# Kernel optimization log

Hardware: AMD Instinct MI355X
Metric: run time of the kernel (lower is better)

## Reference

```python
import jax, jax.numpy as jnp
import numpy as np

K = 3
PAD = 1
DG = 4
GN_GROUPS = 32
EPS = 1e-5


def deform_conv2d(x, offset, weight):
    # x: [B,C,H,W], offset: [B,DG*2*K*K,H,W] (mmcv layout: per group, per kernel tap, (dy,dx))
    B, C, H, W = x.shape
    KK = K * K
    cg = C // DG
    dt = x.dtype
    off = offset.reshape(B, DG, KK, 2, H, W)
    dy, dx = off[:, :, :, 0], off[:, :, :, 1]  # [B,DG,KK,H,W]
    ky, kx = jnp.meshgrid(jnp.arange(K), jnp.arange(K), indexing='ij')
    ky = ky.reshape(KK).astype(dt)
    kx = kx.reshape(KK).astype(dt)
    hh = jnp.arange(H, dtype=dt)
    ww = jnp.arange(W, dtype=dt)
    # sampling coords: p0 + p_k + offset (stride 1, dilation 1)
    y = hh[None, None, None, :, None] - PAD + ky[None, None, :, None, None] + dy
    xs = ww[None, None, None, None, :] - PAD + kx[None, None, :, None, None] + dx
    y0 = jnp.floor(y)
    x0 = jnp.floor(xs)
    wy1 = y - y0
    wx1 = xs - x0
    xg = x.reshape(B, DG, cg, H * W)

    def corner(yi, xi):
        # zero padding outside the feature map
        valid = (yi >= 0) & (yi < H) & (xi >= 0) & (xi < W)
        yc = jnp.clip(yi, 0, H - 1).astype(jnp.int32)
        xc = jnp.clip(xi, 0, W - 1).astype(jnp.int32)
        idx = (yc * W + xc).reshape(B, DG, KK * H * W)
        v = jax.vmap(jax.vmap(lambda xf, ix: xf[:, ix]))(xg, idx)  # [B,DG,cg,KK*H*W]
        v = v.reshape(B, DG, cg, KK, H, W)
        return v * valid.astype(dt)[:, :, None]

    col = (corner(y0, x0) * ((1 - wy1) * (1 - wx1))[:, :, None]
           + corner(y0, x0 + 1) * ((1 - wy1) * wx1)[:, :, None]
           + corner(y0 + 1, x0) * (wy1 * (1 - wx1))[:, :, None]
           + corner(y0 + 1, x0 + 1) * (wy1 * wx1)[:, :, None])  # [B,DG,cg,KK,H,W]
    col = col.reshape(B, C, KK, H, W)
    O = weight.shape[0]
    return jnp.einsum('ock,bckhw->bohw', weight.reshape(O, C, KK), col)


def group_norm(x, gamma, beta):
    B, C, H, W = x.shape
    xg = x.reshape(B, GN_GROUPS, -1)
    m = xg.mean(-1, keepdims=True)
    v = xg.var(-1, keepdims=True)
    xn = ((xg - m) * jax.lax.rsqrt(v + EPS)).reshape(B, C, H, W)
    return xn * gamma[None, :, None, None] + beta[None, :, None, None]


def setup_inputs() -> dict:
    key = jax.random.key(0)
    k1, k2, k3, k4 = jax.random.split(key, 4)
    B, C, H, W = 4, 256, 64, 64
    x = jax.random.normal(k1, (B, C, H, W), dtype=jnp.float32)
    shape = jax.random.normal(k2, (B, 4, H, W), dtype=jnp.float32)
    w_offset = jax.random.normal(k3, (DG * 2 * K * K, 4), dtype=jnp.float32) * 0.01
    w_deform = jax.random.normal(k4, (C, C, K, K), dtype=jnp.float32) * 0.01
    gamma = jnp.ones((C,), jnp.float32)
    beta = jnp.zeros((C,), jnp.float32)
    return {"x": x, "shape": shape, "w_offset": w_offset, "w_deform": w_deform, "gamma": gamma, "beta": beta}


def reference(x, shape, w_offset, w_deform, gamma, beta):
    # conv_offset: 1x1 conv on detached `shape`
    offset = jnp.einsum('oi,bihw->bohw', w_offset, jax.lax.stop_gradient(shape))
    out = deform_conv2d(x, offset, w_deform)
    return jax.nn.relu(group_norm(out, gamma, beta))
```

## Files before the change

kernel.cpp:

```cpp
#include <hip/hip_runtime.h>
#include <stdint.h>

#define BB   4
#define CCH  256
#define HH   64
#define WWD  64
#define HWSZ 4096
#define DGRP 4
#define CG   64
#define KKN  9
#define KT   2304
#define NND  16384
#define GNG  32
#define EPSV 1e-5f

#define WS_COLT  0
#define WS_WB    75497472
#define WS_G     76677120
#define WS_STATS 93454336
#define WS_PART  93455360

typedef __attribute__((ext_vector_type(8))) short short8;
typedef __attribute__((ext_vector_type(4))) float f32x4;

__device__ inline unsigned short f2bf(float f) {
    union { float f; unsigned u; } v; v.f = f;
    unsigned u = v.u;
    return (unsigned short)((u + 0x7FFFu + ((u >> 16) & 1u)) >> 16);
}

__device__ inline void gl_lds16(const void* g, void* l) {
    __builtin_amdgcn_global_load_lds(
        (const __attribute__((address_space(1))) void*)g,
        (__attribute__((address_space(3))) void*)l,
        16, 0, 0);
}

__global__ __launch_bounds__(256) void wconv_kernel(const float* __restrict__ wd,
                                                    unsigned short* __restrict__ Wb) {
    int idx = blockIdx.x * 256 + threadIdx.x;
    int o = idx / KT;
    int r = idx % KT;
    int kk = r >> 8;
    int c  = r & 255;
    Wb[idx] = f2bf(wd[o * KT + c * KKN + kk]);
}

__global__ __launch_bounds__(256) void col_kernel(const float* __restrict__ x,
                                                  const float* __restrict__ shp,
                                                  const float* __restrict__ woff,
                                                  unsigned short* __restrict__ colT) {
    __shared__ __align__(16) float xt[8 * 8 * 64 * 4];

    int bid   = blockIdx.x;
    int band  = bid & 15;
    int chalf = (bid >> 4) & 1;
    int dg    = (bid >> 5) & 3;
    int b     = bid >> 7;
    int h0    = band * 4;
    int tid   = threadIdx.x;
    int lane  = tid & 63;
    int wv    = tid >> 6;

    const float* xg = x + (size_t)(b * CCH + dg * CG + chalf * 32) * HWSZ;
    #pragma unroll 1
    for (int ii = 0; ii < 8; ++ii) {
        float v[8]; int la[8];
        #pragma unroll
        for (int u = 0; u < 8; ++u) {
            int idx = (ii * 8 + u) * 256 + tid;
            int w = idx & 63;
            int r = (idx >> 6) & 7;
            int j = idx >> 9;
            int gr = min(max(h0 - 2 + r, 0), HH - 1);
            v[u]  = xg[(size_t)j * HWSZ + gr * 64 + w];
            la[u] = ((j >> 2) * 8 + r) * 256 + w * 4 + (j & 3);
        }
        #pragma unroll
        for (int u = 0; u < 8; ++u) xt[la[u]] = v[u];
    }
    __syncthreads();

    int h  = h0 + wv;
    int hw = h * 64 + lane;
    float s0 = shp[(b * 4 + 0) * HWSZ + hw];
    float s1 = shp[(b * 4 + 1) * HWSZ + hw];
    float s2 = shp[(b * 4 + 2) * HWSZ + hw];
    float s3 = shp[(b * 4 + 3) * HWSZ + hw];

    unsigned short* rowp = colT + (size_t)(b * HWSZ + hw) * KT + dg * CG + chalf * 32;
    const char* xtb = (const char*)xt;

    #pragma unroll
    for (int kk = 0; kk < KKN; ++kk) {
        const float* wo = woff + (dg * 18 + kk * 2) * 4;
        float dy = wo[0] * s0 + wo[1] * s1 + wo[2] * s2 + wo[3] * s3;
        float dx = wo[4] * s0 + wo[5] * s1 + wo[6] * s2 + wo[7] * s3;

        int ky = kk / 3, kx = kk % 3;
        float y  = (float)(h - 1 + ky) + dy;
        float xs = (float)(lane - 1 + kx) + dx;
        float y0f = floorf(y), x0f = floorf(xs);
        float wy1 = y - y0f,  wx1 = xs - x0f;
        float wy0 = 1.f - wy1, wx0 = 1.f - wx1;
        int iy0 = (int)y0f, ix0 = (int)x0f;
        int iy1 = iy0 + 1,  ix1 = ix0 + 1;
        bool vy0 = (iy0 >= 0) && (iy0 < HH);
        bool vy1 = (iy1 >= 0) && (iy1 < HH);
        bool vx0 = (ix0 >= 0) && (ix0 < WWD);
        bool vx1 = (ix1 >= 0) && (ix1 < WWD);
        float w00 = (vy0 && vx0) ? wy0 * wx0 : 0.f;
        float w01 = (vy0 && vx1) ? wy0 * wx1 : 0.f;
        float w10 = (vy1 && vx0) ? wy1 * wx0 : 0.f;
        float w11 = (vy1 && vx1) ? wy1 * wx1 : 0.f;
        int cy0 = min(max(iy0, 0), HH - 1);
        int cy1 = min(max(iy1, 0), HH - 1);
        int cx0 = min(max(ix0, 0), WWD - 1);
        int cx1 = min(max(ix1, 0), WWD - 1);
        int ty0 = min(max(cy0 - (h0 - 2), 0), 7);
        int ty1 = min(max(cy1 - (h0 - 2), 0), 7);
        int a00 = (ty0 * 64 + cx0) * 16;
        int a01 = (ty0 * 64 + cx1) * 16;
        int a10 = (ty1 * 64 + cx0) * 16;
        int a11 = (ty1 * 64 + cx1) * 16;

        unsigned short tmp[32];
        #pragma unroll
        for (int c4g = 0; c4g < 8; ++c4g) {
            int base = c4g * 8192;
            const float4 v00 = *(const float4*)(xtb + base + a00);
            const float4 v01 = *(const float4*)(xtb + base + a01);
            const float4 v10 = *(const float4*)(xtb + base + a10);
            const float4 v11 = *(const float4*)(xtb + base + a11);
            float rx = w00 * v00.x + w01 * v01.x + w10 * v10.x + w11 * v11.x;
            float ry = w00 * v00.y + w01 * v01.y + w10 * v10.y + w11 * v11.y;
            float rz = w00 * v00.z + w01 * v01.z + w10 * v10.z + w11 * v11.z;
            float rw = w00 * v00.w + w01 * v01.w + w10 * v10.w + w11 * v11.w;
            tmp[c4g * 4 + 0] = f2bf(rx);
            tmp[c4g * 4 + 1] = f2bf(ry);
            tmp[c4g * 4 + 2] = f2bf(rz);
            tmp[c4g * 4 + 3] = f2bf(rw);
        }
        uint4* dst = (uint4*)(rowp + kk * 256);
        const uint4* src = (const uint4*)tmp;
        dst[0] = src[0];
        dst[1] = src[1];
        dst[2] = src[2];
        dst[3] = src[3];
    }
}

__global__ __launch_bounds__(256) void gemm_kernel(const unsigned short* __restrict__ Wb,
                                                   const unsigned short* __restrict__ colT,
                                                   float* __restrict__ G) {
    __shared__ __align__(16) short As[64 * 32];
    __shared__ __align__(16) short Bs[128 * 32];

    int tid  = threadIdx.x;
    int lane = tid & 63;
    int wv   = tid >> 6;
    int wm   = wv >> 1;
    int wn   = wv & 1;
    int m0   = (blockIdx.x & 3) * 64;
    int n0   = (blockIdx.x >> 2) * 128;

    int erow = tid >> 2;
    int ecol = (tid & 3) * 8;
    const unsigned short* gA = Wb   + (size_t)(m0 + erow) * KT + ecol;
    const unsigned short* gB = colT + (size_t)(n0 + erow) * KT + ecol;
    short* lA = As + tid * 8;
    short* lB = Bs + tid * 8;

    f32x4 acc[2][4] = {};

    int quad = lane >> 4;
    int lrow = lane & 15;

    for (int kt = 0; kt < KT; kt += 32) {
        gl_lds16(gA + kt,            lA);
        gl_lds16(gB + kt,            lB);
        gl_lds16(gB + 64 * KT + kt,  lB + 2048);
        __syncthreads();

        short8 a[2], b[4];
        #pragma unroll
        for (int i = 0; i < 2; ++i)
            a[i] = *(const short8*)&As[(wm * 32 + i * 16 + lrow) * 32 + quad * 8];
        #pragma unroll
        for (int j = 0; j < 4; ++j)
            b[j] = *(const short8*)&Bs[(wn * 64 + j * 16 + lrow) * 32 + quad * 8];
        #pragma unroll
        for (int i = 0; i < 2; ++i)
            #pragma unroll
            for (int j = 0; j < 4; ++j)
                acc[i][j] = __builtin_amdgcn_mfma_f32_16x16x32_bf16(a[i], b[j], acc[i][j], 0, 0, 0);
        __syncthreads();
    }

    #pragma unroll
    for (int i = 0; i < 2; ++i) {
        int m = m0 + wm * 32 + i * 16 + quad * 4;
        #pragma unroll
        for (int j = 0; j < 4; ++j) {
            int n = n0 + wn * 64 + j * 16 + lrow;
            #pragma unroll
            for (int r = 0; r < 4; ++r)
                G[(size_t)(m + r) * NND + n] = acc[i][j][r];
        }
    }
}

__global__ __launch_bounds__(256) void gn_part_kernel(const float* __restrict__ G,
                                                      float* __restrict__ partials) {
    int blk = blockIdx.x;
    int bg  = blk >> 3;
    int o   = blk & 7;
    int b   = bg >> 5;
    int g   = bg & 31;
    const float* row = G + (size_t)(g * 8 + o) * NND + b * HWSZ;
    float s1 = 0.f, s2 = 0.f;
    #pragma unroll
    for (int it = 0; it < 16; ++it) {
        float v = row[it * 256 + threadIdx.x];
        s1 += v;
        s2 += v * v;
    }
    #pragma unroll
    for (int off = 1; off < 64; off <<= 1) {
        s1 += __shfl_xor(s1, off);
        s2 += __shfl_xor(s2, off);
    }
    __shared__ float red[8];
    if ((threadIdx.x & 63) == 0) {
        red[(threadIdx.x >> 6) * 2]     = s1;
        red[(threadIdx.x >> 6) * 2 + 1] = s2;
    }
    __syncthreads();
    if (threadIdx.x == 0) {
        partials[blk * 2]     = red[0] + red[2] + red[4] + red[6];
        partials[blk * 2 + 1] = red[1] + red[3] + red[5] + red[7];
    }
}

__global__ __launch_bounds__(128) void gn_stats_kernel(const float* __restrict__ partials,
                                                       float* __restrict__ stats) {
    int bg = threadIdx.x;
    float t1 = 0.f, t2 = 0.f;
    #pragma unroll
    for (int o = 0; o < 8; ++o) {
        t1 += partials[(bg * 8 + o) * 2];
        t2 += partials[(bg * 8 + o) * 2 + 1];
    }
    const float invN = 1.f / 32768.f;
    float mean = t1 * invN;
    float var  = t2 * invN - mean * mean;
    stats[bg * 2]     = mean;
    stats[bg * 2 + 1] = rsqrtf(var + EPSV);
}

__global__ __launch_bounds__(256) void gn_apply_kernel(const float* __restrict__ G,
                                                       const float* __restrict__ stats,
                                                       const float* __restrict__ gamma,
                                                       const float* __restrict__ beta,
                                                       float* __restrict__ out) {
    int idx = blockIdx.x * 256 + threadIdx.x;
    int hw4 = idx & 1023;
    int o   = (idx >> 10) & 255;
    int b   = idx >> 18;
    int g   = o >> 3;
    float mean = stats[(b * 32 + g) * 2];
    float rstd = stats[(b * 32 + g) * 2 + 1];
    float ga = gamma[o], be = beta[o];
    const float4 v = *(const float4*)&G[(size_t)o * NND + b * HWSZ + hw4 * 4];
    float4 r;
    r.x = fmaxf(0.f, (v.x - mean) * rstd * ga + be);
    r.y = fmaxf(0.f, (v.y - mean) * rstd * ga + be);
    r.z = fmaxf(0.f, (v.z - mean) * rstd * ga + be);
    r.w = fmaxf(0.f, (v.w - mean) * rstd * ga + be);
    *(float4*)&out[(size_t)(b * CCH + o) * HWSZ + hw4 * 4] = r;
}

extern "C" void kernel_launch(void* const* d_in, const int* in_sizes, int n_in,
                              void* d_out, int out_size, void* d_ws, size_t ws_size,
                              hipStream_t stream) {
    const float* x     = (const float*)d_in[0];
    const float* shp   = (const float*)d_in[1];
    const float* woff  = (const float*)d_in[2];
    const float* wdef  = (const float*)d_in[3];
    const float* gamma = (const float*)d_in[4];
    const float* beta  = (const float*)d_in[5];
    float* out = (float*)d_out;

    char* ws = (char*)d_ws;
    unsigned short* colT = (unsigned short*)(ws + WS_COLT);
    unsigned short* Wb   = (unsigned short*)(ws + WS_WB);
    float* G             = (float*)(ws + WS_G);
    float* stats         = (float*)(ws + WS_STATS);
    float* partials      = (float*)(ws + WS_PART);

    wconv_kernel<<<2304, 256, 0, stream>>>(wdef, Wb);
    col_kernel<<<512, 256, 0, stream>>>(x, shp, woff, colT);
    gemm_kernel<<<512, 256, 0, stream>>>(Wb, colT, G);
    gn_part_kernel<<<1024, 256, 0, stream>>>(G, partials);
    gn_stats_kernel<<<1, 128, 0, stream>>>(partials, stats);
    gn_apply_kernel<<<4096, 256, 0, stream>>>(G, stats, gamma, beta, out);
}
```

Before: 164.5 us.

## Retile deform-conv GEMM to full-M 256x64 blocks with K-step 64

The GEMM block now covers all 256 output channels and 64 columns, using 512 threads (8 waves in a 4x2 layout) and a K-step of 64, so each colT column tile is loaded only once instead of four times. The weight tile is reloaded per block, which is cheaper because the weights are small and cache-resident. Halving the number of K iterations also halves the barrier count. In exchange, the grid drops to 256 blocks, which may underfill a 256-CU device, and LDS use grows to about 40KB per block.

```diff
diff --git a/kernel.cpp b/kernel.cpp
--- a/kernel.cpp
+++ b/kernel.cpp
@@ -150,59 +150,61 @@
     }
 }
 
-__global__ __launch_bounds__(256) void gemm_kernel(const unsigned short* __restrict__ Wb,
+__global__ __launch_bounds__(512) void gemm_kernel(const unsigned short* __restrict__ Wb,
                                                    const unsigned short* __restrict__ colT,
                                                    float* __restrict__ G) {
-    __shared__ __align__(16) short As[64 * 32];
-    __shared__ __align__(16) short Bs[128 * 32];
+    __shared__ __align__(16) short As[256 * 64];
+    __shared__ __align__(16) short Bs[64 * 64];
 
     int tid  = threadIdx.x;
     int lane = tid & 63;
     int wv   = tid >> 6;
-    int wm   = wv >> 1;
-    int wn   = wv & 1;
-    int m0   = (blockIdx.x & 3) * 64;
-    int n0   = (blockIdx.x >> 2) * 128;
-
-    int erow = tid >> 2;
-    int ecol = (tid & 3) * 8;
-    const unsigned short* gA = Wb   + (size_t)(m0 + erow) * KT + ecol;
-    const unsigned short* gB = colT + (size_t)(n0 + erow) * KT + ecol;
-    short* lA = As + tid * 8;
-    short* lB = Bs + tid * 8;
-
-    f32x4 acc[2][4] = {};
+    int wm   = wv & 3;
+    int wn   = wv >> 2;
+    int n0   = blockIdx.x * 64;
+
+    int arow = tid >> 3;
+    int ach  = (tid & 7) * 8;
+    const unsigned short* gB = colT + (size_t)(n0 + arow) * KT + ach;
+
+    f32x4 acc[4][2] = {};
 
     int quad = lane >> 4;
     int lrow = lane & 15;
 
-    for (int kt = 0; kt < KT; kt += 32) {
-        gl_lds16(gA + kt,            lA);
-        gl_lds16(gB + kt,            lB);
-        gl_lds16(gB + 64 * KT + kt,  lB + 2048);
+    for (int kt = 0; kt < KT; kt += 64) {
+        #pragma unroll
+        for (int u = 0; u < 4; ++u) {
+            int e = u * 512 + tid;
+            gl_lds16(Wb + (size_t)(u * 64 + arow) * KT + kt + ach, (short*)As + e * 8);
+        }
+        gl_lds16(gB + kt, (short*)Bs + tid * 8);
         __syncthreads();
 
-        short8 a[2], b[4];
-        #pragma unroll
-        for (int i = 0; i < 2; ++i)
-            a[i] = *(const short8*)&As[(wm * 32 + i * 16 + lrow) * 32 + quad * 8];
-        #pragma unroll
-        for (int j = 0; j < 4; ++j)
-            b[j] = *(const short8*)&Bs[(wn * 64 + j * 16 + lrow) * 32 + quad * 8];
-        #pragma unroll
-        for (int i = 0; i < 2; ++i)
+        #pragma unroll
+        for (int kb = 0; kb < 2; ++kb) {
+            short8 a[4], b[2];
             #pragma unroll
-            for (int j = 0; j < 4; ++j)
-                acc[i][j] = __builtin_amdgcn_mfma_f32_16x16x32_bf16(a[i], b[j], acc[i][j], 0, 0, 0);
+            for (int i = 0; i < 4; ++i)
+                a[i] = *(const short8*)&As[(wm * 64 + i * 16 + lrow) * 64 + kb * 32 + quad * 8];
+            #pragma unroll
+            for (int j = 0; j < 2; ++j)
+                b[j] = *(const short8*)&Bs[(wn * 32 + j * 16 + lrow) * 64 + kb * 32 + quad * 8];
+            #pragma unroll
+            for (int i = 0; i < 4; ++i)
+                #pragma unroll
+                for (int j = 0; j < 2; ++j)
+                    acc[i][j] = __builtin_amdgcn_mfma_f32_16x16x32_bf16(a[i], b[j], acc[i][j], 0, 0, 0);
+        }
         __syncthreads();
     }
 
     #pragma unroll
-    for (int i = 0; i < 2; ++i) {
-        int m = m0 + wm * 32 + i * 16 + quad * 4;
-        #pragma unroll
-        for (int j = 0; j < 4; ++j) {
-            int n = n0 + wn * 64 + j * 16 + lrow;
+    for (int i = 0; i < 4; ++i) {
+        int m = wm * 64 + i * 16 + quad * 4;
+        #pragma unroll
+        for (int j = 0; j < 2; ++j) {
+            int n = n0 + wn * 32 + j * 16 + lrow;
             #pragma unroll
             for (int r = 0; r < 4; ++r)
                 G[(size_t)(m + r) * NND + n] = acc[i][j][r];
@@ -300,7 +302,7 @@
 
     wconv_kernel<<<2304, 256, 0, stream>>>(wdef, Wb);
     col_kernel<<<512, 256, 0, stream>>>(x, shp, woff, colT);
-    gemm_kernel<<<512, 256, 0, stream>>>(Wb, colT, G);
+    gemm_kernel<<<256, 512, 0, stream>>>(Wb, colT, G);
     gn_part_kernel<<<1024, 256, 0, stream>>>(G, partials);
     gn_stats_kernel<<<1, 128, 0, stream>>>(partials, stats);
     gn_apply_kernel<<<4096, 256, 0, stream>>>(G, stats, gamma, beta, out);
```

After: 176.0 us. 1.07x slower.

## Deepen GEMM K-tile to 64 with XOR-swizzled LDS and XCD-aware block mapping

Applied to the files above, without the earlier changes.

The bf16 MFMA GEMM now stages 64-wide K slices per iteration instead of 32, halving the number of barrier pairs per output tile. LDS rows are written and read through an XOR swizzle of the 16-byte slot index to avoid bank conflicts on the short8 fragment reads. Block indices are remapped so that blocks sharing a column tile land on the same XCD, which is meant to improve L2 reuse of colT. LDS usage doubles, which may reduce occupancy.

```diff
diff --git a/kernel.cpp b/kernel.cpp
--- a/kernel.cpp
+++ b/kernel.cpp
@@ -153,47 +153,62 @@
 __global__ __launch_bounds__(256) void gemm_kernel(const unsigned short* __restrict__ Wb,
                                                    const unsigned short* __restrict__ colT,
                                                    float* __restrict__ G) {
-    __shared__ __align__(16) short As[64 * 32];
-    __shared__ __align__(16) short Bs[128 * 32];
+    __shared__ __align__(16) short As[64 * 64];
+    __shared__ __align__(16) short Bs[128 * 64];
 
     int tid  = threadIdx.x;
     int lane = tid & 63;
     int wv   = tid >> 6;
     int wm   = wv >> 1;
     int wn   = wv & 1;
-    int m0   = (blockIdx.x & 3) * 64;
-    int n0   = (blockIdx.x >> 2) * 128;
-
-    int erow = tid >> 2;
-    int ecol = (tid & 3) * 8;
-    const unsigned short* gA = Wb   + (size_t)(m0 + erow) * KT + ecol;
-    const unsigned short* gB = colT + (size_t)(n0 + erow) * KT + ecol;
-    short* lA = As + tid * 8;
-    short* lB = Bs + tid * 8;
+
+    int idx  = blockIdx.x;
+    int xcd  = idx & 7;
+    int j2   = idx >> 3;
+    int n0   = (xcd * 16 + (j2 >> 2)) * 128;
+    int m0   = (j2 & 3) * 64;
+
+    int r_a = tid >> 3;
+    int s_a = tid & 7;
+    int k_a = (s_a ^ (r_a & 7)) * 8;
 
     f32x4 acc[2][4] = {};
 
     int quad = lane >> 4;
     int lrow = lane & 15;
-
-    for (int kt = 0; kt < KT; kt += 32) {
-        gl_lds16(gA + kt,            lA);
-        gl_lds16(gB + kt,            lB);
-        gl_lds16(gB + 64 * KT + kt,  lB + 2048);
+    int sw   = lrow & 7;
+
+    for (int kt = 0; kt < KT; kt += 64) {
+        #pragma unroll
+        for (int u = 0; u < 2; ++u) {
+            int rr = u * 32 + r_a;
+            gl_lds16(Wb + (size_t)(m0 + rr) * KT + kt + k_a,
+                     (short*)As + (u * 256 + tid) * 8);
+        }
+        #pragma unroll
+        for (int u = 0; u < 4; ++u) {
+            int rr = u * 32 + r_a;
+            gl_lds16(colT + (size_t)(n0 + rr) * KT + kt + k_a,
+                     (short*)Bs + (u * 256 + tid) * 8);
+        }
         __syncthreads();
 
-        short8 a[2], b[4];
-        #pragma unroll
-        for (int i = 0; i < 2; ++i)
-            a[i] = *(const short8*)&As[(wm * 32 + i * 16 + lrow) * 32 + quad * 8];
-        #pragma unroll
-        for (int j = 0; j < 4; ++j)
-            b[j] = *(const short8*)&Bs[(wn * 64 + j * 16 + lrow) * 32 + quad * 8];
-        #pragma unroll
-        for (int i = 0; i < 2; ++i)
+        #pragma unroll
+        for (int kb = 0; kb < 2; ++kb) {
+            int slot = (kb * 4 + quad) ^ sw;
+            short8 a[2], b[4];
+            #pragma unroll
+            for (int i = 0; i < 2; ++i)
+                a[i] = *(const short8*)&As[(wm * 32 + i * 16 + lrow) * 64 + slot * 8];
             #pragma unroll
             for (int j = 0; j < 4; ++j)
-                acc[i][j] = __builtin_amdgcn_mfma_f32_16x16x32_bf16(a[i], b[j], acc[i][j], 0, 0, 0);
+                b[j] = *(const short8*)&Bs[(wn * 64 + j * 16 + lrow) * 64 + slot * 8];
+            #pragma unroll
+            for (int i = 0; i < 2; ++i)
+                #pragma unroll
+                for (int j = 0; j < 4; ++j)
+                    acc[i][j] = __builtin_amdgcn_mfma_f32_16x16x32_bf16(a[i], b[j], acc[i][j], 0, 0, 0);
+        }
         __syncthreads();
     }
 
```

New measurement: 151.9 us. -7.7%, faster.
